# Optimization experiments

Measured on AMD Instinct MI355X. Metric: run time of the kernel, lower is better.

Reference implementation:

```python
import jax, jax.numpy as jnp
import numpy as np

K = 1024
D = 512
DECAY = 0.99


def setup_inputs() -> dict:
    key = jax.random.key(0)
    k1, k2, k3 = jax.random.split(key, 3)
    z_e_x = jax.random.normal(k1, (64, 256, D), dtype=jnp.float32)
    codebook = jax.random.normal(k2, (K, D), dtype=jnp.float32)
    ema_count = jnp.ones((K,), dtype=jnp.float32)
    ema_w = jax.random.normal(k3, (K, D), dtype=jnp.float32)
    return {"z_e_x": z_e_x, "codebook": codebook,
            "ema_count": ema_count, "ema_w": ema_w}


def reference(z_e_x, codebook, ema_count, ema_w):
    # --- vector quantization: nearest codebook entry (squared L2) ---
    flat = z_e_x.reshape(-1, D)                       # [N, D]
    cb_sqr = jnp.sum(codebook ** 2, axis=1)           # [K]
    in_sqr = jnp.sum(flat ** 2, axis=1, keepdims=True)  # [N, 1]
    distances = (cb_sqr[None, :] + in_sqr) - 2.0 * (flat @ codebook.T)  # [N, K]
    indices = jnp.argmin(distances, axis=1)           # [N] int

    # straight-through codes from current codebook
    z_q_x = codebook[indices].reshape(z_e_x.shape)

    # --- EMA codebook update (training branch) ---
    counts = jnp.zeros((K,), dtype=flat.dtype).at[indices].add(1.0)       # sum of one-hots
    new_ema_count = DECAY * ema_count + (1.0 - DECAY) * counts
    dw = jnp.zeros((K, D), dtype=flat.dtype).at[indices].add(flat)        # one_hot.T @ flat
    new_ema_w = DECAY * ema_w + (1.0 - DECAY) * dw
    new_embedding = new_ema_w / new_ema_count[:, None]

    # codes from the updated codebook
    z_q_x_bar = new_embedding[indices].reshape(z_e_x.shape)

    return (z_q_x, z_q_x_bar, new_embedding, new_ema_count, new_ema_w)
```

## Files before the change

kernel.cpp:

```cpp
#include <hip/hip_runtime.h>

typedef _Float16 half8  __attribute__((ext_vector_type(8)));
typedef float    f32x4  __attribute__((ext_vector_type(4)));

constexpr int K_CODES = 1024;
constexpr int D_DIM   = 512;
constexpr float DECAY = 0.99f;
constexpr float OMD   = 0.01f;
constexpr float LO_SCALE = 2048.0f;
constexpr float INV_LO   = 1.0f / 2048.0f;

constexpr int BM = 128;
constexpr int BN = 128;
constexpr int BK = 32;
constexpr int TILE = BM * BK;
constexpr int NPART = K_CODES / BN;
constexpr int CHUNK = 32;

__global__ __launch_bounds__(256)
void prepsplit_kernel(const float* __restrict__ A, const float* __restrict__ cb,
                      float* __restrict__ cbsqr, float* __restrict__ counts,
                      _Float16* __restrict__ ah, _Float16* __restrict__ al,
                      _Float16* __restrict__ bh, _Float16* __restrict__ bl,
                      int nA) {
    int b = blockIdx.x;
    if (b < nA) {
        size_t i8 = ((size_t)b * 256 + threadIdx.x) * 8;
        f32x4 v0 = *reinterpret_cast<const f32x4*>(&A[i8]);
        f32x4 v1 = *reinterpret_cast<const f32x4*>(&A[i8 + 4]);
        half8 h, l;
        #pragma unroll
        for (int j = 0; j < 4; ++j) {
            _Float16 hh = (_Float16)v0[j];
            h[j] = hh;
            l[j] = (_Float16)((v0[j] - (float)hh) * LO_SCALE);
        }
        #pragma unroll
        for (int j = 0; j < 4; ++j) {
            _Float16 hh = (_Float16)v1[j];
            h[4 + j] = hh;
            l[4 + j] = (_Float16)((v1[j] - (float)hh) * LO_SCALE);
        }
        *reinterpret_cast<half8*>(&ah[i8]) = h;
        *reinterpret_cast<half8*>(&al[i8]) = l;
    } else {
        int w    = threadIdx.x >> 6;
        int lane = threadIdx.x & 63;
        int k = (b - nA) * 4 + w;
        size_t base = (size_t)k * D_DIM + lane * 8;
        f32x4 v0 = *reinterpret_cast<const f32x4*>(&cb[base]);
        f32x4 v1 = *reinterpret_cast<const f32x4*>(&cb[base + 4]);
        half8 h, l;
        float s = 0.f;
        #pragma unroll
        for (int j = 0; j < 4; ++j) {
            s += v0[j] * v0[j];
            _Float16 hh = (_Float16)v0[j];
            h[j] = hh;
            l[j] = (_Float16)((v0[j] - (float)hh) * LO_SCALE);
        }
        #pragma unroll
        for (int j = 0; j < 4; ++j) {
            s += v1[j] * v1[j];
            _Float16 hh = (_Float16)v1[j];
            h[4 + j] = hh;
            l[4 + j] = (_Float16)((v1[j] - (float)hh) * LO_SCALE);
        }
        *reinterpret_cast<half8*>(&bh[base]) = h;
        *reinterpret_cast<half8*>(&bl[base]) = l;
        #pragma unroll
        for (int off = 32; off > 0; off >>= 1) s += __shfl_down(s, off);
        if (lane == 0) { cbsqr[k] = s; counts[k] = 0.f; }
    }
}

__global__ __launch_bounds__(256, 2)
void argmin_mfma(const _Float16* __restrict__ Ah,
                 const _Float16* __restrict__ Al,
                 const _Float16* __restrict__ Bh,
                 const _Float16* __restrict__ Bl,
                 const float* __restrict__ cbsqr,
                 float* __restrict__ pval,
                 int*   __restrict__ pidx) {
    __shared__ _Float16 Ahs[2][TILE];
    __shared__ _Float16 Als[2][TILE];
    __shared__ _Float16 Bhs[2][TILE];
    __shared__ _Float16 Bls[2][TILE];
    __shared__ float    sv[2][BM];
    __shared__ int      si[2][BM];

    const int tid  = threadIdx.x;
    const int lane = tid & 63;
    const int wid  = tid >> 6;
    const int wr = wid >> 1, wc = wid & 1;
    const int lq = lane >> 4;
    const int lr = lane & 15;

    const int row0  = blockIdx.x * BM;
    const int cbase = blockIdx.y * BN;

    f32x4 acc_h[4][4], acc_c[4][4];
    #pragma unroll
    for (int m = 0; m < 4; ++m)
        #pragma unroll
        for (int n = 0; n < 4; ++n) {
            acc_h[m][n] = f32x4{0.f, 0.f, 0.f, 0.f};
            acc_c[m][n] = f32x4{0.f, 0.f, 0.f, 0.f};
        }

    auto stage = [&](int buf, int d0) {
        #pragma unroll
        for (int it = 0; it < 2; ++it) {
            int p = it * 4096 + wid * 1024 + lane * 16;
            int row  = p >> 6;
            int cpos = (p >> 4) & 3;
            int sc   = cpos ^ ((row ^ (row >> 2)) & 3);
            size_t aoff = (size_t)(row0 + row) * D_DIM + d0 + sc * 8;
            size_t boff = (size_t)(cbase + row) * D_DIM + d0 + sc * 8;
            int dst = it * 2048 + wid * 512;
            __builtin_amdgcn_global_load_lds(
                (const __attribute__((address_space(1))) void*)(Ah + aoff),
                (__attribute__((address_space(3))) void*)(&Ahs[buf][dst]), 16, 0, 0);
            __builtin_amdgcn_global_load_lds(
                (const __attribute__((address_space(1))) void*)(Al + aoff),
                (__attribute__((address_space(3))) void*)(&Als[buf][dst]), 16, 0, 0);
            __builtin_amdgcn_global_load_lds(
                (const __attribute__((address_space(1))) void*)(Bh + boff),
                (__attribute__((address_space(3))) void*)(&Bhs[buf][dst]), 16, 0, 0);
            __builtin_amdgcn_global_load_lds(
                (const __attribute__((address_space(1))) void*)(Bl + boff),
                (__attribute__((address_space(3))) void*)(&Bls[buf][dst]), 16, 0, 0);
        }
    };

    stage(0, 0);
    __syncthreads();

    constexpr int NSTEP = D_DIM / BK;
    for (int t = 0; t < NSTEP; ++t) {
        const int buf = t & 1;
        if (t + 1 < NSTEP) {
            stage(buf ^ 1, (t + 1) * BK);
            asm volatile("s_waitcnt vmcnt(8)" ::: "memory");
        } else {
            asm volatile("s_waitcnt vmcnt(0)" ::: "memory");
        }
        __builtin_amdgcn_sched_barrier(0);
        __builtin_amdgcn_s_barrier();

        half8 bh[4], bl[4];
        #pragma unroll
        for (int n = 0; n < 4; ++n) {
            int rB  = wc * 64 + n * 16 + lr;
            int pos = lq ^ ((rB ^ (rB >> 2)) & 3);
            bh[n] = *reinterpret_cast<const half8*>(&Bhs[buf][rB * 32 + pos * 8]);
            bl[n] = *reinterpret_cast<const half8*>(&Bls[buf][rB * 32 + pos * 8]);
        }
        #pragma unroll
        for (int m = 0; m < 4; ++m) {
            int rA  = wr * 64 + m * 16 + lr;
            int pos = lq ^ ((rA ^ (rA >> 2)) & 3);
            half8 ah = *reinterpret_cast<const half8*>(&Ahs[buf][rA * 32 + pos * 8]);
            half8 al = *reinterpret_cast<const half8*>(&Als[buf][rA * 32 + pos * 8]);
            #pragma unroll
            for (int n = 0; n < 4; ++n) {
                acc_h[m][n] = __builtin_amdgcn_mfma_f32_16x16x32_f16(ah, bh[n], acc_h[m][n], 0, 0, 0);
                acc_c[m][n] = __builtin_amdgcn_mfma_f32_16x16x32_f16(ah, bl[n], acc_c[m][n], 0, 0, 0);
                acc_c[m][n] = __builtin_amdgcn_mfma_f32_16x16x32_f16(al, bh[n], acc_c[m][n], 0, 0, 0);
            }
        }
        __builtin_amdgcn_s_barrier();
    }

    float cs[4];
    #pragma unroll
    for (int n = 0; n < 4; ++n) cs[n] = cbsqr[cbase + wc * 64 + n * 16 + lr];

    #pragma unroll
    for (int m = 0; m < 4; ++m) {
        #pragma unroll
        for (int q = 0; q < 4; ++q) {
            float bv = 3.4e38f;
            int   bi = 0;
            #pragma unroll
            for (int n = 0; n < 4; ++n) {
                float d = cs[n] - 2.0f * acc_h[m][n][q] - (2.0f * INV_LO) * acc_c[m][n][q];
                int   c = cbase + wc * 64 + n * 16 + lr;
                if (d < bv) { bv = d; bi = c; }
            }
            #pragma unroll
            for (int off = 1; off < 16; off <<= 1) {
                float v2 = __shfl_xor(bv, off);
                int   i2 = __shfl_xor(bi, off);
                if (v2 < bv || (v2 == bv && i2 < bi)) { bv = v2; bi = i2; }
            }
            if (lr == 0) {
                int prow = wr * 64 + m * 16 + lq * 4 + q;
                sv[wc][prow] = bv;
                si[wc][prow] = bi;
            }
        }
    }
    __syncthreads();
    if (tid < BM) {
        float v0 = sv[0][tid], v1 = sv[1][tid];
        int   i0 = si[0][tid], i1 = si[1][tid];
        float bv = (v1 < v0) ? v1 : v0;
        int   bi = (v1 < v0) ? i1 : i0;
        pval[(size_t)(row0 + tid) * NPART + blockIdx.y] = bv;
        pidx[(size_t)(row0 + tid) * NPART + blockIdx.y] = bi;
    }
}

__global__ __launch_bounds__(256)
void combine_kernel(const float* __restrict__ pval, const int* __restrict__ pidx,
                    int* __restrict__ indices, float* __restrict__ counts, int N) {
    int r = blockIdx.x * 256 + threadIdx.x;
    if (r >= N) return;
    float bv = pval[(size_t)r * NPART];
    int   bi = pidx[(size_t)r * NPART];
    #pragma unroll
    for (int p = 1; p < NPART; ++p) {
        float v = pval[(size_t)r * NPART + p];
        int  ii = pidx[(size_t)r * NPART + p];
        if (v < bv) { bv = v; bi = ii; }
    }
    indices[r] = bi;
    atomicAdd(&counts[bi], 1.0f);
}

__global__ __launch_bounds__(256)
void scan_kernel(const float* __restrict__ counts,
                 int* __restrict__ offs, int* __restrict__ cursor) {
    __shared__ int part[256];
    int t = threadIdx.x;
    int c[4], s = 0;
    #pragma unroll
    for (int j = 0; j < 4; ++j) { c[j] = (int)counts[t * 4 + j]; s += c[j]; }
    part[t] = s;
    __syncthreads();
    for (int off = 1; off < 256; off <<= 1) {
        int v   = part[t];
        int add = (t >= off) ? part[t - off] : 0;
        __syncthreads();
        part[t] = v + add;
        __syncthreads();
    }
    int run = part[t] - s;
    #pragma unroll
    for (int j = 0; j < 4; ++j) {
        offs[t * 4 + j]   = run;
        cursor[t * 4 + j] = run;
        run += c[j];
    }
    if (t == 255) offs[K_CODES] = part[255];
}

__global__ __launch_bounds__(256)
void zeroscatter_kernel(const int* __restrict__ indices, int* __restrict__ cursor,
                        int* __restrict__ packed, float4* __restrict__ dw,
                        int N, int nzero) {
    int b = blockIdx.x;
    if (b < nzero) {
        dw[b * 256 + threadIdx.x] = make_float4(0.f, 0.f, 0.f, 0.f);
    } else {
        int r = (b - nzero) * 256 + threadIdx.x;
        if (r >= N) return;
        int k = indices[r];
        int pos = atomicAdd(&cursor[k], 1);
        packed[pos] = (k << 16) | r;
    }
}

__global__ __launch_bounds__(128)
void chunksum_kernel(const float* __restrict__ flat, const int* __restrict__ packed,
                     float* __restrict__ dw, int N) {
    __shared__ int ent[CHUNK + 1];
    const int t = threadIdx.x;
    const int base = blockIdx.x * CHUNK;
    const int cnt = min(CHUNK, N - base);
    if (t < cnt) ent[t] = packed[base + t];
    if (t == cnt) ent[t] = -1;
    __syncthreads();

    f32x4 acc = {0.f, 0.f, 0.f, 0.f};
    for (int i0 = 0; i0 < cnt; i0 += 8) {
        const int m = min(8, cnt - i0);
        f32x4 v[8];
        #pragma unroll
        for (int j = 0; j < 8; ++j) {
            if (j < m) {
                int r = ent[i0 + j] & 0xFFFF;
                v[j] = *reinterpret_cast<const f32x4*>(&flat[(size_t)r * D_DIM + t * 4]);
            }
        }
        #pragma unroll
        for (int j = 0; j < 8; ++j) {
            if (j < m) {
                acc[0] += v[j][0]; acc[1] += v[j][1];
                acc[2] += v[j][2]; acc[3] += v[j][3];
                int k = ent[i0 + j] >> 16;
                if ((ent[i0 + j + 1] >> 16) != k) {
                    float* p = &dw[(size_t)k * D_DIM + t * 4];
                    atomicAdd(p + 0, acc[0]);
                    atomicAdd(p + 1, acc[1]);
                    atomicAdd(p + 2, acc[2]);
                    atomicAdd(p + 3, acc[3]);
                    acc = f32x4{0.f, 0.f, 0.f, 0.f};
                }
            }
        }
    }
}

__global__ __launch_bounds__(256)
void tail_kernel(const float* __restrict__ codebook,
                 const float* __restrict__ ema_count, const float* __restrict__ ema_w,
                 const float* __restrict__ counts, const float* __restrict__ dw,
                 const int* __restrict__ indices,
                 float* __restrict__ new_emb, float* __restrict__ new_count,
                 float* __restrict__ new_ema_w,
                 float* __restrict__ zq, float* __restrict__ zqb, int nfin) {
    int b = blockIdx.x;
    if (b < nfin) {
        int gid = b * 256 + threadIdx.x;
        int k = gid >> 7;
        int d = (gid & 127) * 4;
        float nc = DECAY * ema_count[k] + OMD * counts[k];
        size_t off = (size_t)k * D_DIM + d;
        f32x4 w  = *reinterpret_cast<const f32x4*>(&ema_w[off]);
        f32x4 dv = *reinterpret_cast<const f32x4*>(&dw[off]);
        f32x4 nw, ne;
        float inv = 1.0f / nc;
        #pragma unroll
        for (int j = 0; j < 4; ++j) {
            nw[j] = DECAY * w[j] + OMD * dv[j];
            ne[j] = nw[j] * inv;
        }
        *reinterpret_cast<f32x4*>(&new_ema_w[off]) = nw;
        *reinterpret_cast<f32x4*>(&new_emb[off])   = ne;
        if ((gid & 127) == 0) new_count[k] = nc;
    } else {
        int gid = (b - nfin) * 256 + threadIdx.x;
        int r = gid >> 7;
        int d = (gid & 127) * 4;
        int k = indices[r];
        size_t src = (size_t)k * D_DIM + d;
        size_t dst = (size_t)r * D_DIM + d;
        float nc = DECAY * ema_count[k] + OMD * counts[k];
        float inv = 1.0f / nc;
        f32x4 w  = *reinterpret_cast<const f32x4*>(&ema_w[src]);
        f32x4 dv = *reinterpret_cast<const f32x4*>(&dw[src]);
        f32x4 zb;
        #pragma unroll
        for (int j = 0; j < 4; ++j) zb[j] = (DECAY * w[j] + OMD * dv[j]) * inv;
        *reinterpret_cast<f32x4*>(&zqb[dst]) = zb;
        *reinterpret_cast<f32x4*>(&zq[dst])  = *reinterpret_cast<const f32x4*>(&codebook[src]);
    }
}

extern "C" void kernel_launch(void* const* d_in, const int* in_sizes, int n_in,
                              void* d_out, int out_size, void* d_ws, size_t ws_size,
                              hipStream_t stream) {
    const float* z_e_x     = (const float*)d_in[0];
    const float* codebook  = (const float*)d_in[1];
    const float* ema_count = (const float*)d_in[2];
    const float* ema_w     = (const float*)d_in[3];

    const int N = in_sizes[0] / D_DIM;

    float* out = (float*)d_out;
    float* z_q_x     = out;
    float* z_q_x_bar = z_q_x + (size_t)N * D_DIM;
    float* new_emb   = z_q_x_bar + (size_t)N * D_DIM;
    float* new_count = new_emb + (size_t)K_CODES * D_DIM;
    float* new_ema_w = new_count + K_CODES;

    _Float16* Ahp = (_Float16*)z_q_x_bar;
    _Float16* Alp = Ahp + (size_t)N * D_DIM;

    char* ws = (char*)d_ws;
    int*   indices = (int*)ws;
    float* cbsqr   = (float*)(ws + (size_t)N * 4);
    float* pval    = cbsqr + K_CODES;
    int*   pidx    = (int*)(pval + (size_t)N * NPART);
    float* counts  = (float*)(pidx + (size_t)N * NPART);
    _Float16* bh   = (_Float16*)(counts + K_CODES);
    _Float16* bl   = bh + (size_t)K_CODES * D_DIM;
    float* dw      = (float*)bh;
    int*   offs    = (int*)(bl + (size_t)K_CODES * D_DIM);
    int*   cursor  = offs + K_CODES + 1;
    int*   packed  = cursor + K_CODES;

    const int nA = (N * D_DIM / 8) / 256;
    prepsplit_kernel<<<nA + K_CODES / 4, 256, 0, stream>>>(
        z_e_x, codebook, cbsqr, counts, Ahp, Alp, bh, bl, nA);

    dim3 g_argmin(N / BM, K_CODES / BN);
    argmin_mfma<<<g_argmin, 256, 0, stream>>>(Ahp, Alp, bh, bl, cbsqr, pval, pidx);

    combine_kernel<<<(N + 255) / 256, 256, 0, stream>>>(pval, pidx, indices, counts, N);

    scan_kernel<<<1, 256, 0, stream>>>(counts, offs, cursor);

    const int nzero = (K_CODES * D_DIM / 4) / 256;
    zeroscatter_kernel<<<nzero + (N + 255) / 256, 256, 0, stream>>>(
        indices, cursor, packed, (float4*)dw, N, nzero);

    chunksum_kernel<<<(N + CHUNK - 1) / CHUNK, 128, 0, stream>>>(z_e_x, packed, dw, N);

    const int nfin = (K_CODES * D_DIM / 4) / 256;
    tail_kernel<<<nfin + (N * D_DIM / 4) / 256, 256, 0, stream>>>(
        codebook, ema_count, ema_w, counts, dw, indices,
        new_emb, new_count, new_ema_w, z_q_x, z_q_x_bar, nfin);
}
```

Measured before the change: 136.8 us.

## Merge argmin partials with 64-bit atomicMin and fuse combine into scan kernel

Each argmin block now packs its per-row best distance (as an order-preserving unsigned key) together with the index into a 64-bit value and applies atomicMin to a per-row slot, replacing the partial-value/index arrays and the separate combine kernel. A single-block kernel then extracts indices, builds the histogram in shared memory, and does the prefix scan, which removes one launch and the global float atomics on counts. The min-key buffer is initialised inside the prep kernel. The trade-off is that one 256-thread block now serially walks all N rows, and the argmin kernel issues global 64-bit atomics.

```diff
diff --git a/kernel.cpp b/kernel.cpp
--- a/kernel.cpp
+++ b/kernel.cpp
@@ -2,6 +2,7 @@
 
 typedef _Float16 half8  __attribute__((ext_vector_type(8)));
 typedef float    f32x4  __attribute__((ext_vector_type(4)));
+typedef unsigned long long u64;
 
 constexpr int K_CODES = 1024;
 constexpr int D_DIM   = 512;
@@ -14,15 +15,14 @@
 constexpr int BN = 128;
 constexpr int BK = 32;
 constexpr int TILE = BM * BK;
-constexpr int NPART = K_CODES / BN;
 constexpr int CHUNK = 32;
 
 __global__ __launch_bounds__(256)
 void prepsplit_kernel(const float* __restrict__ A, const float* __restrict__ cb,
-                      float* __restrict__ cbsqr, float* __restrict__ counts,
+                      float* __restrict__ cbsqr, u64* __restrict__ minkey,
                       _Float16* __restrict__ ah, _Float16* __restrict__ al,
                       _Float16* __restrict__ bh, _Float16* __restrict__ bl,
-                      int nA) {
+                      int nA, int nB) {
     int b = blockIdx.x;
     if (b < nA) {
         size_t i8 = ((size_t)b * 256 + threadIdx.x) * 8;
@@ -43,7 +43,7 @@
         }
         *reinterpret_cast<half8*>(&ah[i8]) = h;
         *reinterpret_cast<half8*>(&al[i8]) = l;
-    } else {
+    } else if (b < nA + nB) {
         int w    = threadIdx.x >> 6;
         int lane = threadIdx.x & 63;
         int k = (b - nA) * 4 + w;
@@ -70,7 +70,10 @@
         *reinterpret_cast<half8*>(&bl[base]) = l;
         #pragma unroll
         for (int off = 32; off > 0; off >>= 1) s += __shfl_down(s, off);
-        if (lane == 0) { cbsqr[k] = s; counts[k] = 0.f; }
+        if (lane == 0) cbsqr[k] = s;
+    } else {
+        int i = (b - nA - nB) * 256 + threadIdx.x;
+        minkey[i] = ~0ull;
     }
 }
 
@@ -80,8 +83,7 @@
                  const _Float16* __restrict__ Bh,
                  const _Float16* __restrict__ Bl,
                  const float* __restrict__ cbsqr,
-                 float* __restrict__ pval,
-                 int*   __restrict__ pidx) {
+                 u64* __restrict__ minkey) {
     __shared__ _Float16 Ahs[2][TILE];
     __shared__ _Float16 Als[2][TILE];
     __shared__ _Float16 Bhs[2][TILE];
@@ -207,36 +209,32 @@
         int   i0 = si[0][tid], i1 = si[1][tid];
         float bv = (v1 < v0) ? v1 : v0;
         int   bi = (v1 < v0) ? i1 : i0;
-        pval[(size_t)(row0 + tid) * NPART + blockIdx.y] = bv;
-        pidx[(size_t)(row0 + tid) * NPART + blockIdx.y] = bi;
+        unsigned u = __float_as_uint(bv);
+        unsigned k32 = ((int)u >= 0) ? (u ^ 0x80000000u) : ~u;
+        u64 key = ((u64)k32 << 32) | (unsigned)bi;
+        atomicMin(&minkey[row0 + tid], key);
     }
 }
 
 __global__ __launch_bounds__(256)
-void combine_kernel(const float* __restrict__ pval, const int* __restrict__ pidx,
-                    int* __restrict__ indices, float* __restrict__ counts, int N) {
-    int r = blockIdx.x * 256 + threadIdx.x;
-    if (r >= N) return;
-    float bv = pval[(size_t)r * NPART];
-    int   bi = pidx[(size_t)r * NPART];
-    #pragma unroll
-    for (int p = 1; p < NPART; ++p) {
-        float v = pval[(size_t)r * NPART + p];
-        int  ii = pidx[(size_t)r * NPART + p];
-        if (v < bv) { bv = v; bi = ii; }
-    }
-    indices[r] = bi;
-    atomicAdd(&counts[bi], 1.0f);
-}
-
-__global__ __launch_bounds__(256)
-void scan_kernel(const float* __restrict__ counts,
-                 int* __restrict__ offs, int* __restrict__ cursor) {
+void postargmin_kernel(const u64* __restrict__ minkey, int* __restrict__ indices,
+                       float* __restrict__ counts, int* __restrict__ offs,
+                       int* __restrict__ cursor, int N) {
+    __shared__ int hist[K_CODES];
     __shared__ int part[256];
     int t = threadIdx.x;
+    #pragma unroll
+    for (int j = 0; j < K_CODES / 256; ++j) hist[t + j * 256] = 0;
+    __syncthreads();
+    for (int i = t; i < N; i += 256) {
+        int idx = (int)(unsigned)(minkey[i] & 0xFFFFFFFFull);
+        indices[i] = idx;
+        atomicAdd(&hist[idx], 1);
+    }
+    __syncthreads();
     int c[4], s = 0;
     #pragma unroll
-    for (int j = 0; j < 4; ++j) { c[j] = (int)counts[t * 4 + j]; s += c[j]; }
+    for (int j = 0; j < 4; ++j) { c[j] = hist[t * 4 + j]; s += c[j]; }
     part[t] = s;
     __syncthreads();
     for (int off = 1; off < 256; off <<= 1) {
@@ -251,6 +249,7 @@
     for (int j = 0; j < 4; ++j) {
         offs[t * 4 + j]   = run;
         cursor[t * 4 + j] = run;
+        counts[t * 4 + j] = (float)c[j];
         run += c[j];
     }
     if (t == 255) offs[K_CODES] = part[255];
@@ -382,9 +381,8 @@
     char* ws = (char*)d_ws;
     int*   indices = (int*)ws;
     float* cbsqr   = (float*)(ws + (size_t)N * 4);
-    float* pval    = cbsqr + K_CODES;
-    int*   pidx    = (int*)(pval + (size_t)N * NPART);
-    float* counts  = (float*)(pidx + (size_t)N * NPART);
+    u64*   minkey  = (u64*)(cbsqr + K_CODES);
+    float* counts  = (float*)(minkey + N);
     _Float16* bh   = (_Float16*)(counts + K_CODES);
     _Float16* bl   = bh + (size_t)K_CODES * D_DIM;
     float* dw      = (float*)bh;
@@ -393,15 +391,15 @@
     int*   packed  = cursor + K_CODES;
 
     const int nA = (N * D_DIM / 8) / 256;
-    prepsplit_kernel<<<nA + K_CODES / 4, 256, 0, stream>>>(
-        z_e_x, codebook, cbsqr, counts, Ahp, Alp, bh, bl, nA);
+    const int nB = K_CODES / 4;
+    const int nI = N / 256;
+    prepsplit_kernel<<<nA + nB + nI, 256, 0, stream>>>(
+        z_e_x, codebook, cbsqr, minkey, Ahp, Alp, bh, bl, nA, nB);
 
     dim3 g_argmin(N / BM, K_CODES / BN);
-    argmin_mfma<<<g_argmin, 256, 0, stream>>>(Ahp, Alp, bh, bl, cbsqr, pval, pidx);
-
-    combine_kernel<<<(N + 255) / 256, 256, 0, stream>>>(pval, pidx, indices, counts, N);
-
-    scan_kernel<<<1, 256, 0, stream>>>(counts, offs, cursor);
+    argmin_mfma<<<g_argmin, 256, 0, stream>>>(Ahp, Alp, bh, bl, cbsqr, minkey);
+
+    postargmin_kernel<<<1, 256, 0, stream>>>(minkey, indices, counts, offs, cursor, N);
 
     const int nzero = (K_CODES * D_DIM / 4) / 256;
     zeroscatter_kernel<<<nzero + (N + 255) / 256, 256, 0, stream>>>(
```

After: 141.4 us. 1.03x slower.
